# Performance work log

Hardware: AMD Instinct MI355X
Metric: run time of the kernel (lower is better)

Reference implementation:

```python
import jax, jax.numpy as jnp
import numpy as np

BITS = 50

def _xor(a, b):
    # binary XOR on {0,1} floats: a + b - 2ab
    return a + b - 2.0 * a * b

def _maj(a, b, c):
    # majority (carry-out of a full adder) on {0,1} floats
    return a * b + a * c + b * c - 2.0 * a * b * c

def setup_inputs() -> dict:
    key = jax.random.key(0)
    kA, kB = jax.random.split(key)
    N = 1_000_000
    A = jax.random.randint(kA, (N, BITS), 0, 2).astype(jnp.float32)
    B = jax.random.randint(kB, (N, BITS), 0, 2).astype(jnp.float32)
    return {"A": A, "B": B}

def reference(A, B):
    """A - B via two's complement ripple-carry: A + NOT(B) + 1, LSB first.
    Returns (result [..., 50], borrow [..., 1])."""
    not_b = 1.0 - B                      # VecNOT
    # scan over the 50 bits (sequential carry dependency)
    a_bits = jnp.moveaxis(A, -1, 0)      # [50, N]
    b_bits = jnp.moveaxis(not_b, -1, 0)  # [50, N]
    c0 = jnp.ones(A.shape[:-1], dtype=A.dtype)  # initial carry = 1

    def step(c, ab):
        a, b = ab
        s = _xor(_xor(a, b), c)          # FullAdder sum
        c_next = _maj(a, b, c)           # FullAdder carry
        return c_next, s

    c_final, sums = jax.lax.scan(step, c0, (a_bits, b_bits))
    result = jnp.moveaxis(sums, 0, -1)   # [N, 50]
    borrow = (1.0 - c_final)[..., None]  # borrow_not(carry), [N, 1]
    return result, borrow
```

## Files before the change

### kernel.cpp

```cpp
#include <hip/hip_runtime.h>


constexpr int BITS = 50;
constexpr unsigned long long MASK50 = (1ULL << BITS) - 1ULL;

__device__ inline unsigned long long shfl64(unsigned long long v, int src) {
    int lo = __shfl((int)(unsigned)(v & 0xffffffffULL), src, 64);
    int hi = __shfl((int)(unsigned)(v >> 32), src, 64);
    return ((unsigned long long)(unsigned)hi << 32) | (unsigned long long)(unsigned)lo;
}

__global__ __launch_bounds__(256) void Subtractor50Bit_kernel(
    const float* __restrict__ A, const float* __restrict__ B,
    float* __restrict__ out, int N)
{
    const int lane = threadIdx.x & 63;
    const int wv   = threadIdx.x >> 6;
    const long long waveIdx = (long long)blockIdx.x * 4 + wv;
    const long long rowBase = waveIdx * 64;
    if (rowBase >= N) return;

    if (rowBase + 64 <= N) {
        const long long eBase = rowBase * BITS;
        const float* pa = A + eBase + lane;
        const float* pb = B + eBase + lane;

        float fa[BITS], fb[BITS];
        #pragma unroll
        for (int j = 0; j < BITS; ++j) fa[j] = pa[(long long)j * 64];
        #pragma unroll
        for (int j = 0; j < BITS; ++j) fb[j] = pb[(long long)j * 64];

        unsigned long long wa = 0, wb = 0;
        #pragma unroll
        for (int j = 0; j < BITS; ++j) {
            unsigned long long ma = __ballot(fa[j] != 0.0f);
            unsigned long long mb = __ballot(fb[j] != 0.0f);
            if (lane == j) { wa = ma; wb = mb; }
        }

        const int p0   = BITS * lane;
        const int idx0 = p0 >> 6;
        const int sh   = p0 & 63;
        unsigned long long a0 = shfl64(wa, idx0);
        unsigned long long a1 = shfl64(wa, idx0 + 1);
        unsigned long long b0 = shfl64(wb, idx0);
        unsigned long long b1 = shfl64(wb, idx0 + 1);

        unsigned long long av = a0 >> sh;
        unsigned long long bv = b0 >> sh;
        if (sh > 64 - BITS) {
            av |= a1 << (64 - sh);
            bv |= b1 << (64 - sh);
        }
        av &= MASK50;
        bv &= MASK50;

        unsigned long long diff = (av - bv) & MASK50;
        float borrow = (av < bv) ? 1.0f : 0.0f;

        #pragma unroll
        for (int j = 0; j < BITS; ++j) {
            int local = j * 64 + lane;
            int r     = local / BITS;
            int bit   = local - r * BITS;
            unsigned long long dr = shfl64(diff, r);
            out[eBase + local] = (float)((dr >> bit) & 1ULL);
        }
        out[(long long)N * BITS + rowBase + lane] = borrow;
    } else {
        long long r = rowBase + lane;
        if (r < N) {
            unsigned long long av = 0, bv = 0;
            for (int k = 0; k < BITS; ++k) {
                av |= (unsigned long long)(A[r * BITS + k] != 0.0f) << k;
                bv |= (unsigned long long)(B[r * BITS + k] != 0.0f) << k;
            }
            unsigned long long diff = (av - bv) & MASK50;
            for (int k = 0; k < BITS; ++k)
                out[r * BITS + k] = (float)((diff >> k) & 1ULL);
            out[(long long)N * BITS + r] = (av < bv) ? 1.0f : 0.0f;
        }
    }
}

extern "C" void kernel_launch(void* const* d_in, const int* in_sizes, int n_in,
                              void* d_out, int out_size, void* d_ws, size_t ws_size,
                              hipStream_t stream) {
    const float* A = (const float*)d_in[0];
    const float* B = (const float*)d_in[1];
    float* out = (float*)d_out;
    const int N = in_sizes[0] / BITS;

    const int waves  = (N + 63) / 64;
    const int blocks = (waves + 3) / 4;
    Subtractor50Bit_kernel<<<blocks, 256, 0, stream>>>(A, B, out, N);
}
```

Baseline: 449.6 us.

## Vectorize loads/stores as float2 and use nontemporal stores

Loads A and B as float2, which halves the number of load instructions. Even and odd bits are collected by separate ballots and re-interleaved with a bit-spread (Morton) step. Output is written as 64-bit pairs of floats built by bit selection, using nontemporal stores to avoid polluting the cache. This cuts the instruction count for memory traffic in a bandwidth-bound kernel, at the cost of more shuffles and bit manipulation.

```diff
diff --git a/kernel.cpp b/kernel.cpp
--- a/kernel.cpp
+++ b/kernel.cpp
@@ -8,6 +8,15 @@
     int lo = __shfl((int)(unsigned)(v & 0xffffffffULL), src, 64);
     int hi = __shfl((int)(unsigned)(v >> 32), src, 64);
     return ((unsigned long long)(unsigned)hi << 32) | (unsigned long long)(unsigned)lo;
+}
+
+__device__ inline unsigned long long spread2(unsigned long long x) {
+    x = (x | (x << 16)) & 0x0000FFFF0000FFFFULL;
+    x = (x | (x << 8))  & 0x00FF00FF00FF00FFULL;
+    x = (x | (x << 4))  & 0x0F0F0F0F0F0F0F0FULL;
+    x = (x | (x << 2))  & 0x3333333333333333ULL;
+    x = (x | (x << 1))  & 0x5555555555555555ULL;
+    return x;
 }
 
 __global__ __launch_bounds__(256) void Subtractor50Bit_kernel(
@@ -22,52 +31,73 @@
 
     if (rowBase + 64 <= N) {
         const long long eBase = rowBase * BITS;
-        const float* pa = A + eBase + lane;
-        const float* pb = B + eBase + lane;
+        const float2* pa = (const float2*)(A + eBase) + lane;
+        const float2* pb = (const float2*)(B + eBase) + lane;
 
-        float fa[BITS], fb[BITS];
+        float2 fa[25], fb[25];
         #pragma unroll
-        for (int j = 0; j < BITS; ++j) fa[j] = pa[(long long)j * 64];
+        for (int t = 0; t < 25; ++t) fa[t] = pa[t * 64];
         #pragma unroll
-        for (int j = 0; j < BITS; ++j) fb[j] = pb[(long long)j * 64];
+        for (int t = 0; t < 25; ++t) fb[t] = pb[t * 64];
 
         unsigned long long wa = 0, wb = 0;
+        const int  lane31 = lane & 31;
+        const bool isLo   = lane < 32;
         #pragma unroll
-        for (int j = 0; j < BITS; ++j) {
-            unsigned long long ma = __ballot(fa[j] != 0.0f);
-            unsigned long long mb = __ballot(fb[j] != 0.0f);
-            if (lane == j) { wa = ma; wb = mb; }
+        for (int t = 0; t < 25; ++t) {
+            unsigned long long aE = __ballot(fa[t].x != 0.0f);
+            unsigned long long aO = __ballot(fa[t].y != 0.0f);
+            unsigned long long bE = __ballot(fb[t].x != 0.0f);
+            unsigned long long bO = __ballot(fb[t].y != 0.0f);
+            if (lane31 == t) {
+                wa = isLo ? aE : aO;
+                wb = isLo ? bE : bO;
+            }
         }
 
-        const int p0   = BITS * lane;
-        const int idx0 = p0 >> 6;
-        const int sh   = p0 & 63;
-        unsigned long long a0 = shfl64(wa, idx0);
-        unsigned long long a1 = shfl64(wa, idx0 + 1);
-        unsigned long long b0 = shfl64(wb, idx0);
-        unsigned long long b1 = shfl64(wb, idx0 + 1);
+        const int p0 = 25 * lane;
+        const int w0 = p0 >> 6;
+        const int sh = p0 & 63;
 
-        unsigned long long av = a0 >> sh;
-        unsigned long long bv = b0 >> sh;
-        if (sh > 64 - BITS) {
-            av |= a1 << (64 - sh);
-            bv |= b1 << (64 - sh);
+        unsigned long long aE0 = shfl64(wa, w0);
+        unsigned long long aE1 = shfl64(wa, w0 + 1);
+        unsigned long long aO0 = shfl64(wa, 32 + w0);
+        unsigned long long aO1 = shfl64(wa, 33 + w0);
+        unsigned long long bE0 = shfl64(wb, w0);
+        unsigned long long bE1 = shfl64(wb, w0 + 1);
+        unsigned long long bO0 = shfl64(wb, 32 + w0);
+        unsigned long long bO1 = shfl64(wb, 33 + w0);
+
+        unsigned long long evA = aE0 >> sh, odA = aO0 >> sh;
+        unsigned long long evB = bE0 >> sh, odB = bO0 >> sh;
+        if (sh > 39) {
+            const int c = 64 - sh;
+            evA |= aE1 << c; odA |= aO1 << c;
+            evB |= bE1 << c; odB |= bO1 << c;
         }
-        av &= MASK50;
-        bv &= MASK50;
+        const unsigned long long M25 = (1ULL << 25) - 1ULL;
+        evA &= M25; odA &= M25; evB &= M25; odB &= M25;
+
+        unsigned long long av = spread2(evA) | (spread2(odA) << 1);
+        unsigned long long bv = spread2(evB) | (spread2(odB) << 1);
 
         unsigned long long diff = (av - bv) & MASK50;
         float borrow = (av < bv) ? 1.0f : 0.0f;
 
+        unsigned long long* po = (unsigned long long*)(out + eBase);
         #pragma unroll
-        for (int j = 0; j < BITS; ++j) {
-            int local = j * 64 + lane;
-            int r     = local / BITS;
-            int bit   = local - r * BITS;
+        for (int j = 0; j < 25; ++j) {
+            int q = j * 64 + lane;
+            int r = q / 25;
+            int k = 2 * (q - r * 25);
             unsigned long long dr = shfl64(diff, r);
-            out[eBase + local] = (float)((dr >> bit) & 1ULL);
+            unsigned long long t2 = dr >> k;
+            unsigned long long o =
+                  ((t2 & 1ULL) ? 0x000000003F800000ULL : 0ULL)
+                | ((t2 & 2ULL) ? 0x3F80000000000000ULL : 0ULL);
+            __builtin_nontemporal_store(o, po + q);
         }
-        out[(long long)N * BITS + rowBase + lane] = borrow;
+        __builtin_nontemporal_store(borrow, out + (long long)N * BITS + rowBase + lane);
     } else {
         long long r = rowBase + lane;
         if (r < N) {
```

Result: no change. 458.0 us (+1.9%).

## Stage rows through LDS with direct global-to-LDS loads and vectorized output

Applied to the files above, without the earlier changes.

Replaces the per-element strided loads, the ballot-based bit packing and the 50 shuffle rounds with direct global_load_lds copies of each 64-row tile into shared memory. Each lane then reads its own row as float2 pairs, packs the bits by testing the exponent bit, writes its result bits back into LDS, and the tile is stored with 16-byte vector writes. Blocks shrink to a single wave with 25.6KB of LDS each, so the kernel depends on LDS occupancy and on issuing enough memory traffic from one wave at a time. The exponent-bit test assumes the inputs are exactly 0.0 or 1.0.

```diff
diff --git a/kernel.cpp b/kernel.cpp
--- a/kernel.cpp
+++ b/kernel.cpp
@@ -4,69 +4,87 @@
 constexpr int BITS = 50;
 constexpr unsigned long long MASK50 = (1ULL << BITS) - 1ULL;
 
-__device__ inline unsigned long long shfl64(unsigned long long v, int src) {
-    int lo = __shfl((int)(unsigned)(v & 0xffffffffULL), src, 64);
-    int hi = __shfl((int)(unsigned)(v >> 32), src, 64);
-    return ((unsigned long long)(unsigned)hi << 32) | (unsigned long long)(unsigned)lo;
+__device__ __forceinline__ void gl_lds16(const float* g, float* l) {
+    __builtin_amdgcn_global_load_lds(
+        (const __attribute__((address_space(1))) void*)g,
+        (__attribute__((address_space(3))) void*)l, 16, 0, 0);
+}
+__device__ __forceinline__ void gl_lds4(const float* g, float* l) {
+    __builtin_amdgcn_global_load_lds(
+        (const __attribute__((address_space(1))) void*)g,
+        (__attribute__((address_space(3))) void*)l, 4, 0, 0);
 }
 
-__global__ __launch_bounds__(256) void Subtractor50Bit_kernel(
+__global__ __launch_bounds__(64) void Subtractor50Bit_kernel(
     const float* __restrict__ A, const float* __restrict__ B,
     float* __restrict__ out, int N)
 {
-    const int lane = threadIdx.x & 63;
-    const int wv   = threadIdx.x >> 6;
-    const long long waveIdx = (long long)blockIdx.x * 4 + wv;
-    const long long rowBase = waveIdx * 64;
+    __shared__ float sA[3200];
+    __shared__ float sB[3200];
+
+    const int lane = threadIdx.x;
+    const long long rowBase = (long long)blockIdx.x * 64;
     if (rowBase >= N) return;
 
     if (rowBase + 64 <= N) {
         const long long eBase = rowBase * BITS;
-        const float* pa = A + eBase + lane;
-        const float* pb = B + eBase + lane;
+        const float* ga = A + eBase;
+        const float* gb = B + eBase;
 
-        float fa[BITS], fb[BITS];
         #pragma unroll
-        for (int j = 0; j < BITS; ++j) fa[j] = pa[(long long)j * 64];
+        for (int j = 0; j < 12; ++j) gl_lds16(ga + 256 * j + 4 * lane, &sA[256 * j]);
+        gl_lds4(ga + 3072 + lane, &sA[3072]);
+        gl_lds4(ga + 3136 + lane, &sA[3136]);
         #pragma unroll
-        for (int j = 0; j < BITS; ++j) fb[j] = pb[(long long)j * 64];
+        for (int j = 0; j < 12; ++j) gl_lds16(gb + 256 * j + 4 * lane, &sB[256 * j]);
+        gl_lds4(gb + 3072 + lane, &sB[3072]);
+        gl_lds4(gb + 3136 + lane, &sB[3136]);
 
-        unsigned long long wa = 0, wb = 0;
+        asm volatile("s_waitcnt vmcnt(0)" ::: "memory");
+        __builtin_amdgcn_sched_barrier(0);
+
+        const float2* rA = (const float2*)sA + 25 * lane;
+        const float2* rB = (const float2*)sB + 25 * lane;
+        unsigned alo = 0, ahi = 0, blo = 0, bhi = 0;
         #pragma unroll
-        for (int j = 0; j < BITS; ++j) {
-            unsigned long long ma = __ballot(fa[j] != 0.0f);
-            unsigned long long mb = __ballot(fb[j] != 0.0f);
-            if (lane == j) { wa = ma; wb = mb; }
+        for (int j = 0; j < 25; ++j) {
+            float2 va = rA[j];
+            float2 vb = rB[j];
+            unsigned a0 = (__float_as_uint(va.x) >> 23) & 1u;
+            unsigned a1 = (__float_as_uint(va.y) >> 23) & 1u;
+            unsigned b0 = (__float_as_uint(vb.x) >> 23) & 1u;
+            unsigned b1 = (__float_as_uint(vb.y) >> 23) & 1u;
+            if (j < 16) {
+                alo |= a0 << (2 * j); alo |= a1 << (2 * j + 1);
+                blo |= b0 << (2 * j); blo |= b1 << (2 * j + 1);
+            } else {
+                ahi |= a0 << (2 * j - 32); ahi |= a1 << (2 * j - 31);
+                bhi |= b0 << (2 * j - 32); bhi |= b1 << (2 * j - 31);
+            }
         }
-
-        const int p0   = BITS * lane;
-        const int idx0 = p0 >> 6;
-        const int sh   = p0 & 63;
-        unsigned long long a0 = shfl64(wa, idx0);
-        unsigned long long a1 = shfl64(wa, idx0 + 1);
-        unsigned long long b0 = shfl64(wb, idx0);
-        unsigned long long b1 = shfl64(wb, idx0 + 1);
-
-        unsigned long long av = a0 >> sh;
-        unsigned long long bv = b0 >> sh;
-        if (sh > 64 - BITS) {
-            av |= a1 << (64 - sh);
-            bv |= b1 << (64 - sh);
-        }
-        av &= MASK50;
-        bv &= MASK50;
+        unsigned long long av = ((unsigned long long)ahi << 32) | alo;
+        unsigned long long bv = ((unsigned long long)bhi << 32) | blo;
 
         unsigned long long diff = (av - bv) & MASK50;
         float borrow = (av < bv) ? 1.0f : 0.0f;
 
+        float2* wO = (float2*)sA + 25 * lane;
         #pragma unroll
-        for (int j = 0; j < BITS; ++j) {
-            int local = j * 64 + lane;
-            int r     = local / BITS;
-            int bit   = local - r * BITS;
-            unsigned long long dr = shfl64(diff, r);
-            out[eBase + local] = (float)((dr >> bit) & 1ULL);
+        for (int j = 0; j < 25; ++j) {
+            float2 o;
+            o.x = (float)(unsigned)((diff >> (2 * j)) & 1ULL);
+            o.y = (float)(unsigned)((diff >> (2 * j + 1)) & 1ULL);
+            wO[j] = o;
         }
+
+        const float4* sO4 = (const float4*)sA;
+        float4* go4 = (float4*)(out + eBase);
+        #pragma unroll
+        for (int j = 0; j < 12; ++j) go4[64 * j + lane] = sO4[64 * j + lane];
+        const float2* sO2 = (const float2*)(sA + 3072);
+        float2* go2 = (float2*)(out + eBase + 3072);
+        go2[lane] = sO2[lane];
+
         out[(long long)N * BITS + rowBase + lane] = borrow;
     } else {
         long long r = rowBase + lane;
@@ -92,7 +110,6 @@
     float* out = (float*)d_out;
     const int N = in_sizes[0] / BITS;
 
-    const int waves  = (N + 63) / 64;
-    const int blocks = (waves + 3) / 4;
-    Subtractor50Bit_kernel<<<blocks, 256, 0, stream>>>(A, B, out, N);
+    const int blocks = (N + 63) / 64;
+    Subtractor50Bit_kernel<<<blocks, 64, 0, stream>>>(A, B, out, N);
 }
```

After: 448.8 us. No clear change (-0.2%).

## Process two rows per thread with float4 loads instead of wave ballot/shuffle

Applied to the files above, without the earlier changes.

Replaces the wave-cooperative layout (coalesced strided loads, ballot to pack bits, 64-bit shuffles to redistribute) with a per-thread scheme where each thread owns two adjacent rows (400 contiguous bytes) and reads and writes them with float4 vectors. Bits are extracted from the float exponent bit 23, which relies on inputs being exactly 0.0 or 1.0. This removes the many ballot and shuffle instructions, but each thread now touches a large contiguous span, so per-instruction coalescing across lanes is worse and register pressure rises.

```diff
diff --git a/kernel.cpp b/kernel.cpp
--- a/kernel.cpp
+++ b/kernel.cpp
@@ -4,83 +4,88 @@
 constexpr int BITS = 50;
 constexpr unsigned long long MASK50 = (1ULL << BITS) - 1ULL;
 
-__device__ inline unsigned long long shfl64(unsigned long long v, int src) {
-    int lo = __shfl((int)(unsigned)(v & 0xffffffffULL), src, 64);
-    int hi = __shfl((int)(unsigned)(v >> 32), src, 64);
-    return ((unsigned long long)(unsigned)hi << 32) | (unsigned long long)(unsigned)lo;
+__device__ __forceinline__ void accbit(unsigned bit, int e,
+    unsigned& lo0, unsigned& hi0, unsigned& lo1, unsigned& hi1)
+{
+    if (e < 32)      lo0 |= bit << e;
+    else if (e < 50) hi0 |= bit << (e - 32);
+    else if (e < 82) lo1 |= bit << (e - 50);
+    else             hi1 |= bit << (e - 82);
+}
+
+__device__ __forceinline__ float dbit(unsigned long long d0,
+                                      unsigned long long d1, int e)
+{
+    unsigned long long d = (e < 50) ? d0 : d1;
+    int k = (e < 50) ? e : e - 50;
+    return (float)((unsigned)(d >> k) & 1u);
 }
 
 __global__ __launch_bounds__(256) void Subtractor50Bit_kernel(
     const float* __restrict__ A, const float* __restrict__ B,
     float* __restrict__ out, int N)
 {
-    const int lane = threadIdx.x & 63;
-    const int wv   = threadIdx.x >> 6;
-    const long long waveIdx = (long long)blockIdx.x * 4 + wv;
-    const long long rowBase = waveIdx * 64;
-    if (rowBase >= N) return;
+    const long long t  = (long long)blockIdx.x * 256 + threadIdx.x;
+    const long long r0 = 2 * t;
+    if (r0 >= N) return;
 
-    if (rowBase + 64 <= N) {
-        const long long eBase = rowBase * BITS;
-        const float* pa = A + eBase + lane;
-        const float* pb = B + eBase + lane;
+    if (r0 + 2 <= N) {
+        const float4* pa = (const float4*)(A + r0 * BITS);
+        const float4* pb = (const float4*)(B + r0 * BITS);
 
-        float fa[BITS], fb[BITS];
+        unsigned alo0 = 0, ahi0 = 0, alo1 = 0, ahi1 = 0;
+        unsigned blo0 = 0, bhi0 = 0, blo1 = 0, bhi1 = 0;
+
         #pragma unroll
-        for (int j = 0; j < BITS; ++j) fa[j] = pa[(long long)j * 64];
-        #pragma unroll
-        for (int j = 0; j < BITS; ++j) fb[j] = pb[(long long)j * 64];
-
-        unsigned long long wa = 0, wb = 0;
-        #pragma unroll
-        for (int j = 0; j < BITS; ++j) {
-            unsigned long long ma = __ballot(fa[j] != 0.0f);
-            unsigned long long mb = __ballot(fb[j] != 0.0f);
-            if (lane == j) { wa = ma; wb = mb; }
+        for (int j = 0; j < 25; ++j) {
+            float4 va = pa[j];
+            float4 vb = pb[j];
+            accbit((__float_as_uint(va.x) >> 23) & 1u, 4*j+0, alo0, ahi0, alo1, ahi1);
+            accbit((__float_as_uint(va.y) >> 23) & 1u, 4*j+1, alo0, ahi0, alo1, ahi1);
+            accbit((__float_as_uint(va.z) >> 23) & 1u, 4*j+2, alo0, ahi0, alo1, ahi1);
+            accbit((__float_as_uint(va.w) >> 23) & 1u, 4*j+3, alo0, ahi0, alo1, ahi1);
+            accbit((__float_as_uint(vb.x) >> 23) & 1u, 4*j+0, blo0, bhi0, blo1, bhi1);
+            accbit((__float_as_uint(vb.y) >> 23) & 1u, 4*j+1, blo0, bhi0, blo1, bhi1);
+            accbit((__float_as_uint(vb.z) >> 23) & 1u, 4*j+2, blo0, bhi0, blo1, bhi1);
+            accbit((__float_as_uint(vb.w) >> 23) & 1u, 4*j+3, blo0, bhi0, blo1, bhi1);
         }
 
-        const int p0   = BITS * lane;
-        const int idx0 = p0 >> 6;
-        const int sh   = p0 & 63;
-        unsigned long long a0 = shfl64(wa, idx0);
-        unsigned long long a1 = shfl64(wa, idx0 + 1);
-        unsigned long long b0 = shfl64(wb, idx0);
-        unsigned long long b1 = shfl64(wb, idx0 + 1);
+        const unsigned long long av0 = alo0 | ((unsigned long long)ahi0 << 32);
+        const unsigned long long bv0 = blo0 | ((unsigned long long)bhi0 << 32);
+        const unsigned long long av1 = alo1 | ((unsigned long long)ahi1 << 32);
+        const unsigned long long bv1 = blo1 | ((unsigned long long)bhi1 << 32);
 
-        unsigned long long av = a0 >> sh;
-        unsigned long long bv = b0 >> sh;
-        if (sh > 64 - BITS) {
-            av |= a1 << (64 - sh);
-            bv |= b1 << (64 - sh);
+        const unsigned long long d0 = (av0 - bv0) & MASK50;
+        const unsigned long long d1 = (av1 - bv1) & MASK50;
+        const float bw0 = (av0 < bv0) ? 1.0f : 0.0f;
+        const float bw1 = (av1 < bv1) ? 1.0f : 0.0f;
+
+        float4* po = (float4*)(out + r0 * BITS);
+        #pragma unroll
+        for (int j = 0; j < 25; ++j) {
+            float4 o;
+            o.x = dbit(d0, d1, 4*j+0);
+            o.y = dbit(d0, d1, 4*j+1);
+            o.z = dbit(d0, d1, 4*j+2);
+            o.w = dbit(d0, d1, 4*j+3);
+            po[j] = o;
         }
-        av &= MASK50;
-        bv &= MASK50;
 
-        unsigned long long diff = (av - bv) & MASK50;
-        float borrow = (av < bv) ? 1.0f : 0.0f;
-
-        #pragma unroll
-        for (int j = 0; j < BITS; ++j) {
-            int local = j * 64 + lane;
-            int r     = local / BITS;
-            int bit   = local - r * BITS;
-            unsigned long long dr = shfl64(diff, r);
-            out[eBase + local] = (float)((dr >> bit) & 1ULL);
+        float2 bo;
+        bo.x = bw0;
+        bo.y = bw1;
+        *(float2*)(out + (long long)N * BITS + r0) = bo;
+    } else {
+        const long long r = r0;
+        unsigned long long av = 0, bv = 0;
+        for (int k = 0; k < BITS; ++k) {
+            av |= (unsigned long long)(A[r * BITS + k] != 0.0f) << k;
+            bv |= (unsigned long long)(B[r * BITS + k] != 0.0f) << k;
         }
-        out[(long long)N * BITS + rowBase + lane] = borrow;
-    } else {
-        long long r = rowBase + lane;
-        if (r < N) {
-            unsigned long long av = 0, bv = 0;
-            for (int k = 0; k < BITS; ++k) {
-                av |= (unsigned long long)(A[r * BITS + k] != 0.0f) << k;
-                bv |= (unsigned long long)(B[r * BITS + k] != 0.0f) << k;
-            }
-            unsigned long long diff = (av - bv) & MASK50;
-            for (int k = 0; k < BITS; ++k)
-                out[r * BITS + k] = (float)((diff >> k) & 1ULL);
-            out[(long long)N * BITS + r] = (av < bv) ? 1.0f : 0.0f;
-        }
+        const unsigned long long diff = (av - bv) & MASK50;
+        for (int k = 0; k < BITS; ++k)
+            out[r * BITS + k] = (float)((diff >> k) & 1ULL);
+        out[(long long)N * BITS + r] = (av < bv) ? 1.0f : 0.0f;
     }
 }
 
@@ -92,7 +97,7 @@
     float* out = (float*)d_out;
     const int N = in_sizes[0] / BITS;
 
-    const int waves  = (N + 63) / 64;
-    const int blocks = (waves + 3) / 4;
+    const long long pairs  = ((long long)N + 1) / 2;
+    const int       blocks = (int)((pairs + 255) / 256);
     Subtractor50Bit_kernel<<<blocks, 256, 0, stream>>>(A, B, out, N);
 }
```

After: 535.7 us. +19.1%, slower.
